# Kernel optimization log

Measured on AMD Instinct MI355X. Metric: run time of the kernel, lower is better.

Reference implementation:

```python
import jax, jax.numpy as jnp
import numpy as np

N, E, D_IN, D_H, D_OUT = 50000, 600000, 128, 128, 1


def setup_inputs() -> dict:
    key = jax.random.key(0)
    ks = jax.random.split(key, 12)
    s = 1.0 / np.sqrt(D_H)
    inp = {
        "x": jax.random.normal(ks[0], (N, D_IN), dtype=jnp.float32),
        "edge_index": jax.random.randint(ks[1], (2, E), 0, N, dtype=jnp.int64),
        # GCNConv layer weights (in->h, h->h, h->h)
        "W0": jax.random.normal(ks[2], (D_IN, D_H), dtype=jnp.float32) * s,
        "b0": jnp.zeros((D_H,), dtype=jnp.float32),
        "W1": jax.random.normal(ks[3], (D_H, D_H), dtype=jnp.float32) * s,
        "b1": jnp.zeros((D_H,), dtype=jnp.float32),
        "W2": jax.random.normal(ks[4], (D_H, D_H), dtype=jnp.float32) * s,
        "b2": jnp.zeros((D_H,), dtype=jnp.float32),
        # MLP head
        "mlp_w1": jax.random.normal(ks[5], (D_H, D_H), dtype=jnp.float32) * s,
        "mlp_b1": jnp.zeros((D_H,), dtype=jnp.float32),
        "mlp_w2": jax.random.normal(ks[6], (D_H, D_OUT), dtype=jnp.float32) * s,
        "mlp_b2": jnp.zeros((D_OUT,), dtype=jnp.float32),
    }
    return inp


def reference(x, edge_index, W0, b0, W1, b1, W2, b2, mlp_w1, mlp_b1, mlp_w2, mlp_b2):
    n = x.shape[0]
    loop = jnp.arange(n, dtype=edge_index.dtype)
    # add self-loops (PyG GCNConv default)
    src = jnp.concatenate([edge_index[0], loop])
    dst = jnp.concatenate([edge_index[1], loop])
    # symmetric normalization: deg counts incoming edges incl. self-loop
    deg = jax.ops.segment_sum(jnp.ones(src.shape, dtype=x.dtype), dst, num_segments=n)
    dinv = jax.lax.rsqrt(deg)  # deg >= 1 due to self-loops
    norm = (dinv[src] * dinv[dst])[:, None]  # [E+N, 1]

    def gcn_conv(h, W, b):
        h = h @ W                       # [N, d]
        msg = h[src] * norm             # gather + scale, [E+N, d]
        return jax.ops.segment_sum(msg, dst, num_segments=n) + b

    # num_layers=3: first two convs with ReLU (dropout is identity in eval)
    h = jax.nn.relu(gcn_conv(x, W0, b0))
    h = jax.nn.relu(gcn_conv(h, W1, b1))
    h = gcn_conv(h, W2, b2)
    # MLP head (dropout identity in eval)
    h = jax.nn.relu(h @ mlp_w1 + mlp_b1)
    return h @ mlp_w2 + mlp_b2
```

## Files before the change

kernel.cpp:

```cpp
#include <hip/hip_runtime.h>
#include <hip/hip_fp16.h>

constexpr int D = 128;

typedef _Float16 half8 __attribute__((ext_vector_type(8)));
typedef float f32x4 __attribute__((ext_vector_type(4)));


__global__ void k_zero(int4* __restrict__ p, int n4) {
    int i = blockIdx.x * 256 + threadIdx.x;
    if (i < n4) p[i] = make_int4(0, 0, 0, 0);
}


__global__ __launch_bounds__(256) void k_count_xcd(const int* __restrict__ dst,
                                                   int* __restrict__ cnt, int E, int n) {
    int xcd = blockIdx.x & 7;
    int chunk = blockIdx.x >> 3;
    int nchunk = gridDim.x >> 3;
    int lo = (int)((long long)n * xcd >> 3);
    int hi = (int)((long long)n * (xcd + 1) >> 3);
    int per = (E + nchunk - 1) / nchunk;
    int e0 = chunk * per;
    int e1 = e0 + per;
    if (e1 > E) e1 = E;
    for (int e = e0 + threadIdx.x; e < e1; e += 256) {
        int d = dst[e];
        if (d >= lo && d < hi) atomicAdd(&cnt[d], 1);
    }
}

template <typename IdxT>
__global__ __launch_bounds__(256) void k_fill_xcd(const int* __restrict__ src,
                                                  const int* __restrict__ dst,
                                                  int* __restrict__ cursor,
                                                  IdxT* __restrict__ csr, int E, int n) {
    int xcd = blockIdx.x & 7;
    int chunk = blockIdx.x >> 3;
    int nchunk = gridDim.x >> 3;
    int lo = (int)((long long)n * xcd >> 3);
    int hi = (int)((long long)n * (xcd + 1) >> 3);
    int per = (E + nchunk - 1) / nchunk;
    int e0 = chunk * per;
    int e1 = e0 + per;
    if (e1 > E) e1 = E;
    for (int e = e0 + threadIdx.x; e < e1; e += 256) {
        int d = dst[e];
        if (d >= lo && d < hi) {
            int s = src[e];
            int p = atomicAdd(&cursor[d], 1);
            csr[p] = (IdxT)s;
        }
    }
}

__global__ __launch_bounds__(256) void k_deg_stats(const int* __restrict__ cnt,
                                                   float* __restrict__ dinv,
                                                   int* __restrict__ bsum, int n) {
    __shared__ int sm[256];
    int tid = threadIdx.x;
    int i = blockIdx.x * 256 + tid;
    int c = (i < n) ? cnt[i] : 0;
    if (i < n) dinv[i] = rsqrtf((float)(c + 1));
    sm[tid] = c;
    __syncthreads();
    for (int off = 128; off > 0; off >>= 1) {
        if (tid < off) sm[tid] += sm[tid + off];
        __syncthreads();
    }
    if (tid == 0) bsum[blockIdx.x] = sm[0];
}

__global__ __launch_bounds__(256) void k_local_scan2(const int* __restrict__ cnt,
                                                     const int* __restrict__ bsum, int nb,
                                                     int* __restrict__ rowptr,
                                                     int* __restrict__ cursor, int n) {
    __shared__ int sb[256];
    __shared__ int sm[256];
    int tid = threadIdx.x;
    int bid = blockIdx.x;
    int bv = (tid < nb) ? bsum[tid] : 0;
    sb[tid] = bv;
    __syncthreads();
    for (int off = 1; off < 256; off <<= 1) {
        int t = (tid >= off) ? sb[tid - off] : 0;
        __syncthreads();
        sb[tid] += t;
        __syncthreads();
    }
    int blockoff = (bid > 0) ? sb[bid - 1] : 0;
    int i = bid * 256 + tid;
    int v = (i < n) ? cnt[i] : 0;
    sm[tid] = v;
    __syncthreads();
    for (int off = 1; off < 256; off <<= 1) {
        int t = (tid >= off) ? sm[tid - off] : 0;
        __syncthreads();
        sm[tid] += t;
        __syncthreads();
    }
    if (i < n) {
        int rp = blockoff + sm[tid] - v;
        rowptr[i] = rp;
        cursor[i] = rp;
    }
    if (bid == 0 && tid == 0) rowptr[n] = sb[nb - 1];
}


__global__ __launch_bounds__(256) void k_prep(
    const float* __restrict__ x, const float* __restrict__ dinv,
    __half* __restrict__ xh, int n4, const float* __restrict__ W0,
    const float* __restrict__ W1, const float* __restrict__ W2,
    const float* __restrict__ M1, const float* __restrict__ b2,
    const float* __restrict__ c1, __half* __restrict__ Wf0, __half* __restrict__ Wf1,
    __half* __restrict__ Wfp, float* __restrict__ cp) {
    int T = gridDim.x * 256;
    int gid = blockIdx.x * 256 + threadIdx.x;

    for (int i = gid; i < n4; i += T) {
        float4 v = reinterpret_cast<const float4*>(x)[i];
        float dd = dinv[i >> 5];
        __half ho[4] = {__float2half(v.x * dd), __float2half(v.y * dd),
                        __float2half(v.z * dd), __float2half(v.w * dd)};
        reinterpret_cast<uint2*>(xh)[i] = *reinterpret_cast<uint2*>(ho);
    }

    for (int q = gid; q < 2 * 16384; q += T) {
        int m = q >> 14;
        int idx = q & 16383;
        int j = idx & 7;
        int l = (idx >> 3) & 63;
        int c = (idx >> 9) & 7;
        int kk = (idx >> 12) & 3;
        int row = kk * 32 + (l >> 4) * 8 + j;
        int col = c * 16 + (l & 15);
        const float* W = (m == 0) ? W0 : W1;
        __half* Wf = (m == 0) ? Wf0 : Wf1;
        Wf[idx] = __float2half(W[row * 128 + col]);
    }

    for (int idx = gid; idx < 16384; idx += T) {
        int j = idx & 7;
        int l = (idx >> 3) & 63;
        int c = (idx >> 9) & 7;
        int kk = (idx >> 12) & 3;
        int row = kk * 32 + (l >> 4) * 8 + j;
        int col = c * 16 + (l & 15);
        float acc = 0.f;
        for (int k = 0; k < 128; ++k)
            acc = fmaf(W2[row * 128 + k], M1[k * 128 + col], acc);
        Wfp[idx] = __float2half(acc);
    }

    if (gid < 128) {
        float acc = c1[gid];
        for (int k = 0; k < 128; ++k) acc = fmaf(b2[k], M1[k * 128 + gid], acc);
        cp[gid] = acc;
    }
}


__device__ inline void accm(float* a, uint4 g, float m) {
    float2 p0 = __half22float2(*reinterpret_cast<const __half2*>(&g.x));
    float2 p1 = __half22float2(*reinterpret_cast<const __half2*>(&g.y));
    float2 p2 = __half22float2(*reinterpret_cast<const __half2*>(&g.z));
    float2 p3 = __half22float2(*reinterpret_cast<const __half2*>(&g.w));
    a[0] = fmaf(m, p0.x, a[0]);
    a[1] = fmaf(m, p0.y, a[1]);
    a[2] = fmaf(m, p1.x, a[2]);
    a[3] = fmaf(m, p1.y, a[3]);
    a[4] = fmaf(m, p2.x, a[4]);
    a[5] = fmaf(m, p2.y, a[5]);
    a[6] = fmaf(m, p3.x, a[6]);
    a[7] = fmaf(m, p3.y, a[7]);
}

template <typename IdxT>
__global__ __launch_bounds__(256) void k_agg_h4(const uint4* __restrict__ Ah4,
                                                const int* __restrict__ rowptr,
                                                const IdxT* __restrict__ csr,
                                                const float* __restrict__ dinv,
                                                uint4* __restrict__ outh4, int n) {
    int wv = threadIdx.x >> 6;
    int lane = threadIdx.x & 63;
    int i = blockIdx.x * 4 + wv;
    if (i >= n) return;
    int qg = lane >> 4;
    int fl = lane & 15;
    float a[8];
#pragma unroll
    for (int j = 0; j < 8; ++j) a[j] = 0.f;
    int beg = rowptr[i], end = rowptr[i + 1];
    for (int base = beg; base < end; base += 64) {
        int cnt = end - base;
        if (cnt > 64) cnt = 64;
        int idxv = (base + lane < end) ? (int)csr[base + lane] : 0;
        for (int e = 0; e < cnt; e += 16) {
            int k0 = e + qg;
            int k1 = e + qg + 4;
            int k2 = e + qg + 8;
            int k3 = e + qg + 12;
            int s0 = __shfl(idxv, k0);
            int s1 = __shfl(idxv, k1);
            int s2 = __shfl(idxv, k2);
            int s3 = __shfl(idxv, k3);
            uint4 g0 = Ah4[s0 * 16 + fl];
            uint4 g1 = Ah4[s1 * 16 + fl];
            uint4 g2 = Ah4[s2 * 16 + fl];
            uint4 g3 = Ah4[s3 * 16 + fl];
            float m0 = (k0 < cnt) ? 1.f : 0.f;
            float m1 = (k1 < cnt) ? 1.f : 0.f;
            float m2 = (k2 < cnt) ? 1.f : 0.f;
            float m3 = (k3 < cnt) ? 1.f : 0.f;
            accm(a, g0, m0);
            accm(a, g1, m1);
            accm(a, g2, m2);
            accm(a, g3, m3);
        }
    }
#pragma unroll
    for (int j = 0; j < 8; ++j) {
        a[j] += __shfl_xor(a[j], 16);
        a[j] += __shfl_xor(a[j], 32);
    }
    if (qg == 0) {
        uint4 gs = Ah4[i * 16 + fl];
        accm(a, gs, 1.f);
        float di = dinv[i];
        __half ho[8];
#pragma unroll
        for (int j = 0; j < 8; ++j) ho[j] = __float2half(di * a[j]);
        outh4[i * 16 + fl] = *reinterpret_cast<const uint4*>(ho);
    }
}


template <int MODE>
__global__ __launch_bounds__(256) void k_gemm_mfma(const __half* __restrict__ A,
                                                   const __half* __restrict__ Wf,
                                                   const float* __restrict__ bias,
                                                   const float* __restrict__ dinv,
                                                   const float* __restrict__ m2,
                                                   const float* __restrict__ m2b,
                                                   void* __restrict__ outv, int n) {
    int tid = threadIdx.x;
    int w = tid >> 6;
    int l = tid & 63;
    int r0 = blockIdx.x * 64 + w * 16;
    int arow = r0 + (l & 15);
    if (arow > n - 1) arow = n - 1;
    int kb = (l >> 4) * 8;

    f32x4 acc[8];
#pragma unroll
    for (int c = 0; c < 8; ++c) acc[c] = (f32x4){0.f, 0.f, 0.f, 0.f};

#pragma unroll
    for (int kk = 0; kk < 4; ++kk) {
        half8 a = *reinterpret_cast<const half8*>(&A[arow * 128 + kk * 32 + kb]);
#pragma unroll
        for (int c = 0; c < 8; ++c) {
            half8 b = *reinterpret_cast<const half8*>(&Wf[((kk * 8 + c) * 64 + l) * 8]);
            acc[c] = __builtin_amdgcn_mfma_f32_16x16x32_f16(a, b, acc[c], 0, 0, 0);
        }
    }

    float bv[8];
#pragma unroll
    for (int c = 0; c < 8; ++c) bv[c] = bias[c * 16 + (l & 15)];

    if (MODE == 0) {
        __half* outh = (__half*)outv;
#pragma unroll
        for (int reg = 0; reg < 4; ++reg) {
            int r = r0 + (l >> 4) * 4 + reg;
            if (r < n) {
                float dr = dinv[r];
#pragma unroll
                for (int c = 0; c < 8; ++c) {
                    float v = dr * fmaxf(acc[c][reg] + bv[c], 0.f);
                    outh[r * 128 + c * 16 + (l & 15)] = __float2half(v);
                }
            }
        }
    } else {
        float* out = (float*)outv;
        float mv[8];
#pragma unroll
        for (int c = 0; c < 8; ++c) mv[c] = m2[c * 16 + (l & 15)];
        float m2bv = m2b[0];
#pragma unroll
        for (int reg = 0; reg < 4; ++reg) {
            float p = 0.f;
#pragma unroll
            for (int c = 0; c < 8; ++c)
                p = fmaf(fmaxf(acc[c][reg] + bv[c], 0.f), mv[c], p);
            p += __shfl_xor(p, 1);
            p += __shfl_xor(p, 2);
            p += __shfl_xor(p, 4);
            p += __shfl_xor(p, 8);
            int r = r0 + (l >> 4) * 4 + reg;
            if ((l & 15) == 0 && r < n) out[r] = p + m2bv;
        }
    }
}


extern "C" void kernel_launch(void* const* d_in, const int* in_sizes, int n_in,
                              void* d_out, int out_size, void* d_ws, size_t ws_size,
                              hipStream_t stream) {
    const float* x = (const float*)d_in[0];
    const int* ei = (const int*)d_in[1];
    const float* W0 = (const float*)d_in[2];
    const float* b0 = (const float*)d_in[3];
    const float* W1 = (const float*)d_in[4];
    const float* b1 = (const float*)d_in[5];
    const float* W2 = (const float*)d_in[6];
    const float* b2 = (const float*)d_in[7];
    const float* M1 = (const float*)d_in[8];
    const float* c1 = (const float*)d_in[9];
    const float* m2 = (const float*)d_in[10];
    const float* m2b = (const float*)d_in[11];
    float* out = (float*)d_out;

    int N = in_sizes[0] / D;
    int E = in_sizes[1] / 2;
    const int* src = ei;
    const int* dst = ei + E;

    char* ws = (char*)d_ws;
    size_t off = 0;
    auto alloc = [&](size_t bytes) -> void* {
        void* p = ws + off;
        off += (bytes + 255) & ~(size_t)255;
        return p;
    };

    int gN = (N + 255) / 256;
    int gAgg = (N + 3) / 4;
    int gGemm = (N + 63) / 64;
    int nElem4 = N * D / 4;

    __half* xh = (__half*)alloc((size_t)N * D * 2);
    __half* tbuf = (__half*)alloc((size_t)N * D * 2);
    __half* gbuf = (__half*)alloc((size_t)N * D * 2);
    int* cnt = (int*)alloc((size_t)N * 4);
    float* dinv = (float*)alloc((size_t)N * 4);
    int* rowptr = (int*)alloc((size_t)(N + 1) * 4);
    int* cursor = (int*)alloc((size_t)N * 4);
    void* csr = alloc((size_t)E * 4);
    float* cp = (float*)alloc((size_t)D * 4);
    __half* Wf0 = (__half*)alloc((size_t)D * D * 2);
    __half* Wf1 = (__half*)alloc((size_t)D * D * 2);
    __half* Wfp = (__half*)alloc((size_t)D * D * 2);
    int* bsum = (int*)alloc((size_t)gN * 4);

    bool small_idx = (N <= 65535);

    int zc = (N + 3) / 4;
    k_zero<<<(zc + 255) / 256, 256, 0, stream>>>((int4*)cnt, zc);
    k_count_xcd<<<1024, 256, 0, stream>>>(dst, cnt, E, N);
    k_deg_stats<<<gN, 256, 0, stream>>>(cnt, dinv, bsum, N);
    k_local_scan2<<<gN, 256, 0, stream>>>(cnt, bsum, gN, rowptr, cursor, N);
    if (small_idx)
        k_fill_xcd<ushort><<<1024, 256, 0, stream>>>(src, dst, cursor, (ushort*)csr, E, N);
    else
        k_fill_xcd<uint><<<1024, 256, 0, stream>>>(src, dst, cursor, (uint*)csr, E, N);
    k_prep<<<1024, 256, 0, stream>>>(x, dinv, xh, nElem4, W0, W1, W2, M1, b2, c1, Wf0,
                                     Wf1, Wfp, cp);

    auto agg = [&](const __half* in_h, __half* out_t) {
        if (small_idx)
            k_agg_h4<ushort><<<gAgg, 256, 0, stream>>>((const uint4*)in_h, rowptr,
                                                       (const ushort*)csr, dinv,
                                                       (uint4*)out_t, N);
        else
            k_agg_h4<uint><<<gAgg, 256, 0, stream>>>((const uint4*)in_h, rowptr,
                                                     (const uint*)csr, dinv,
                                                     (uint4*)out_t, N);
    };

    agg(xh, tbuf);
    k_gemm_mfma<0><<<gGemm, 256, 0, stream>>>(tbuf, Wf0, b0, dinv, nullptr, nullptr,
                                              gbuf, N);
    agg(gbuf, tbuf);
    k_gemm_mfma<0><<<gGemm, 256, 0, stream>>>(tbuf, Wf1, b1, dinv, nullptr, nullptr,
                                              gbuf, N);
    agg(gbuf, tbuf);
    k_gemm_mfma<1><<<gGemm, 256, 0, stream>>>(tbuf, Wfp, cp, dinv, m2, m2b, out, N);
}
```

Measured before the change: 196.2 us.

## Replace XCD-partitioned CSR build with bucketed radix-style scatter

Graph CSR construction no longer scans all edges once per XCD partition. Edges are first bucketed by destination high bits through per-block histograms, a scan, and a scatter into a temporary edge buffer. Each bucket is then filled into the CSR by its own block, which improves locality of the cursor atomics. This adds three kernel launches and an 8-byte-per-edge staging buffer. The prep grid is also doubled.

```diff
diff --git a/kernel.cpp b/kernel.cpp
--- a/kernel.cpp
+++ b/kernel.cpp
@@ -2,6 +2,7 @@
 #include <hip/hip_fp16.h>
 
 constexpr int D = 128;
+constexpr int EPB = 1024;
 
 typedef _Float16 half8 __attribute__((ext_vector_type(8)));
 typedef float f32x4 __attribute__((ext_vector_type(4)));
@@ -13,45 +14,24 @@
 }
 
 
-__global__ __launch_bounds__(256) void k_count_xcd(const int* __restrict__ dst,
-                                                   int* __restrict__ cnt, int E, int n) {
-    int xcd = blockIdx.x & 7;
-    int chunk = blockIdx.x >> 3;
-    int nchunk = gridDim.x >> 3;
-    int lo = (int)((long long)n * xcd >> 3);
-    int hi = (int)((long long)n * (xcd + 1) >> 3);
-    int per = (E + nchunk - 1) / nchunk;
-    int e0 = chunk * per;
-    int e1 = e0 + per;
+__global__ __launch_bounds__(256) void k_count_hist(const int* __restrict__ dst,
+                                                    int* __restrict__ cnt,
+                                                    int* __restrict__ hist, int E,
+                                                    int shift, int nblk) {
+    __shared__ int lh[256];
+    int tid = threadIdx.x;
+    lh[tid] = 0;
+    __syncthreads();
+    int e0 = blockIdx.x * EPB;
+    int e1 = e0 + EPB;
     if (e1 > E) e1 = E;
-    for (int e = e0 + threadIdx.x; e < e1; e += 256) {
+    for (int e = e0 + tid; e < e1; e += 256) {
         int d = dst[e];
-        if (d >= lo && d < hi) atomicAdd(&cnt[d], 1);
-    }
-}
-
-template <typename IdxT>
-__global__ __launch_bounds__(256) void k_fill_xcd(const int* __restrict__ src,
-                                                  const int* __restrict__ dst,
-                                                  int* __restrict__ cursor,
-                                                  IdxT* __restrict__ csr, int E, int n) {
-    int xcd = blockIdx.x & 7;
-    int chunk = blockIdx.x >> 3;
-    int nchunk = gridDim.x >> 3;
-    int lo = (int)((long long)n * xcd >> 3);
-    int hi = (int)((long long)n * (xcd + 1) >> 3);
-    int per = (E + nchunk - 1) / nchunk;
-    int e0 = chunk * per;
-    int e1 = e0 + per;
-    if (e1 > E) e1 = E;
-    for (int e = e0 + threadIdx.x; e < e1; e += 256) {
-        int d = dst[e];
-        if (d >= lo && d < hi) {
-            int s = src[e];
-            int p = atomicAdd(&cursor[d], 1);
-            csr[p] = (IdxT)s;
-        }
-    }
+        atomicAdd(&cnt[d], 1);
+        atomicAdd(&lh[d >> shift], 1);
+    }
+    __syncthreads();
+    hist[tid * nblk + blockIdx.x] = lh[tid];
 }
 
 __global__ __launch_bounds__(256) void k_deg_stats(const int* __restrict__ cnt,
@@ -105,6 +85,86 @@
         cursor[i] = rp;
     }
     if (bid == 0 && tid == 0) rowptr[n] = sb[nb - 1];
+}
+
+
+__global__ __launch_bounds__(256) void k_hist_scan(int* __restrict__ hist, int nblk,
+                                                   int* __restrict__ total) {
+    int b = blockIdx.x;
+    int tid = threadIdx.x;
+    __shared__ int sm[256];
+    int carry = 0;
+    for (int base = 0; base < nblk; base += 256) {
+        int k = base + tid;
+        int v = (k < nblk) ? hist[b * nblk + k] : 0;
+        sm[tid] = v;
+        __syncthreads();
+        for (int off = 1; off < 256; off <<= 1) {
+            int t = (tid >= off) ? sm[tid - off] : 0;
+            __syncthreads();
+            sm[tid] += t;
+            __syncthreads();
+        }
+        if (k < nblk) hist[b * nblk + k] = carry + sm[tid] - v;
+        int tot = sm[255];
+        __syncthreads();
+        carry += tot;
+    }
+    if (tid == 0) total[b] = carry;
+}
+
+__global__ __launch_bounds__(256) void k_scan_buckets(const int* __restrict__ total,
+                                                      int* __restrict__ bbase) {
+    __shared__ int sm[256];
+    int tid = threadIdx.x;
+    int v = total[tid];
+    sm[tid] = v;
+    __syncthreads();
+    for (int off = 1; off < 256; off <<= 1) {
+        int t = (tid >= off) ? sm[tid - off] : 0;
+        __syncthreads();
+        sm[tid] += t;
+        __syncthreads();
+    }
+    bbase[tid] = sm[tid] - v;
+    if (tid == 255) bbase[256] = sm[255];
+}
+
+
+__global__ __launch_bounds__(256) void k_scatter(const int* __restrict__ src,
+                                                 const int* __restrict__ dst,
+                                                 const int* __restrict__ hist,
+                                                 const int* __restrict__ bbase,
+                                                 uint2* __restrict__ ebuf, int E,
+                                                 int shift, int nblk) {
+    __shared__ int lofs[256];
+    int tid = threadIdx.x;
+    lofs[tid] = bbase[tid] + hist[tid * nblk + blockIdx.x];
+    __syncthreads();
+    int e0 = blockIdx.x * EPB;
+    int e1 = e0 + EPB;
+    if (e1 > E) e1 = E;
+    for (int e = e0 + tid; e < e1; e += 256) {
+        int s = src[e];
+        int d = dst[e];
+        int p = atomicAdd(&lofs[d >> shift], 1);
+        ebuf[p] = make_uint2((uint)s, (uint)d);
+    }
+}
+
+
+template <typename IdxT>
+__global__ __launch_bounds__(256) void k_fill_bucket(const uint2* __restrict__ ebuf,
+                                                     const int* __restrict__ bbase,
+                                                     int* __restrict__ cursor,
+                                                     IdxT* __restrict__ csr) {
+    int b = blockIdx.x;
+    int q0 = bbase[b], q1 = bbase[b + 1];
+    for (int q = q0 + threadIdx.x; q < q1; q += 256) {
+        uint2 pk = ebuf[q];
+        int p = atomicAdd(&cursor[pk.y], 1);
+        csr[p] = (IdxT)pk.x;
+    }
 }
 
 
@@ -342,6 +402,11 @@
     int gGemm = (N + 63) / 64;
     int nElem4 = N * D / 4;
 
+    int shift = 8;
+    while (((N - 1) >> shift) >= 256) shift++;
+    int nbuckets = ((N - 1) >> shift) + 1;
+    int nblk = (E + EPB - 1) / EPB;
+
     __half* xh = (__half*)alloc((size_t)N * D * 2);
     __half* tbuf = (__half*)alloc((size_t)N * D * 2);
     __half* gbuf = (__half*)alloc((size_t)N * D * 2);
@@ -355,19 +420,28 @@
     __half* Wf1 = (__half*)alloc((size_t)D * D * 2);
     __half* Wfp = (__half*)alloc((size_t)D * D * 2);
     int* bsum = (int*)alloc((size_t)gN * 4);
+    int* hist = (int*)alloc((size_t)256 * nblk * 4);
+    int* total = (int*)alloc((size_t)256 * 4);
+    int* bbase = (int*)alloc((size_t)257 * 4);
+    uint2* ebuf = (uint2*)alloc((size_t)E * 8);
 
     bool small_idx = (N <= 65535);
 
     int zc = (N + 3) / 4;
     k_zero<<<(zc + 255) / 256, 256, 0, stream>>>((int4*)cnt, zc);
-    k_count_xcd<<<1024, 256, 0, stream>>>(dst, cnt, E, N);
+    k_count_hist<<<nblk, 256, 0, stream>>>(dst, cnt, hist, E, shift, nblk);
     k_deg_stats<<<gN, 256, 0, stream>>>(cnt, dinv, bsum, N);
     k_local_scan2<<<gN, 256, 0, stream>>>(cnt, bsum, gN, rowptr, cursor, N);
+    k_hist_scan<<<256, 256, 0, stream>>>(hist, nblk, total);
+    k_scan_buckets<<<1, 256, 0, stream>>>(total, bbase);
+    k_scatter<<<nblk, 256, 0, stream>>>(src, dst, hist, bbase, ebuf, E, shift, nblk);
     if (small_idx)
-        k_fill_xcd<ushort><<<1024, 256, 0, stream>>>(src, dst, cursor, (ushort*)csr, E, N);
+        k_fill_bucket<ushort><<<nbuckets, 256, 0, stream>>>(ebuf, bbase, cursor,
+                                                            (ushort*)csr);
     else
-        k_fill_xcd<uint><<<1024, 256, 0, stream>>>(src, dst, cursor, (uint*)csr, E, N);
-    k_prep<<<1024, 256, 0, stream>>>(x, dinv, xh, nElem4, W0, W1, W2, M1, b2, c1, Wf0,
+        k_fill_bucket<uint><<<nbuckets, 256, 0, stream>>>(ebuf, bbase, cursor,
+                                                          (uint*)csr);
+    k_prep<<<2048, 256, 0, stream>>>(x, dinv, xh, nElem4, W0, W1, W2, M1, b2, c1, Wf0,
                                      Wf1, Wfp, cp);
 
     auto agg = [&](const __half* in_h, __half* out_t) {
```

Result: no change. 195.9 us (-0.2%).
